# Optimization experiments

Hardware: AMD Instinct MI355X
Metric: run time of the kernel (lower is better)

Reference implementation:

```python
import jax, jax.numpy as jnp
import numpy as np

N_NODES = 50000
N_EDGES = 800000
IN_CH = 128
HID_CH = 8
OUT_CH = 64
HEADS = 32
NEG_SLOPE = 0.2  # PyG GATConv default


def setup_inputs() -> dict:
    key = jax.random.key(0)
    ks = jax.random.split(key, 12)
    x = jax.random.normal(ks[0], (N_NODES, IN_CH), dtype=jnp.float32)
    # edge_index with no self loops (src != dst), matching PyG's remove_self_loops
    src = jax.random.randint(ks[1], (N_EDGES,), 0, N_NODES)
    off = jax.random.randint(ks[2], (N_EDGES,), 1, N_NODES)
    dst = (src + off) % N_NODES
    edge_index = jnp.stack([src, dst]).astype(jnp.int64)
    s = 0.1
    W1 = jax.random.normal(ks[3], (IN_CH, HEADS * HID_CH), dtype=jnp.float32) * s
    att_src1 = jax.random.normal(ks[4], (HEADS, HID_CH), dtype=jnp.float32) * s
    att_dst1 = jax.random.normal(ks[5], (HEADS, HID_CH), dtype=jnp.float32) * s
    b1 = jnp.zeros((HEADS * HID_CH,), dtype=jnp.float32)
    W2 = jax.random.normal(ks[6], (HEADS * HID_CH, OUT_CH), dtype=jnp.float32) * s
    att_src2 = jax.random.normal(ks[7], (1, OUT_CH), dtype=jnp.float32) * s
    att_dst2 = jax.random.normal(ks[8], (1, OUT_CH), dtype=jnp.float32) * s
    b2 = jnp.zeros((OUT_CH,), dtype=jnp.float32)
    return {"x": x, "edge_index": edge_index, "W1": W1, "att_src1": att_src1,
            "att_dst1": att_dst1, "b1": b1, "W2": W2, "att_src2": att_src2,
            "att_dst2": att_dst2, "b2": b2}


def _gat_conv(x, src, dst, W, a_src, a_dst, bias, concat):
    # Faithful PyG GATConv: linear -> per-edge LeakyReLU score -> segment softmax over dst -> scatter-add
    n = x.shape[0]
    H, C = a_src.shape
    h = (x @ W).reshape(n, H, C)                      # [N,H,C]
    alpha_src = jnp.sum(h * a_src, axis=-1)           # [N,H]
    alpha_dst = jnp.sum(h * a_dst, axis=-1)           # [N,H]
    e = jax.nn.leaky_relu(alpha_src[src] + alpha_dst[dst], negative_slope=NEG_SLOPE)  # [E,H]
    e_max = jax.ops.segment_max(e, dst, num_segments=n)          # every node has a self loop
    ex = jnp.exp(e - e_max[dst])
    denom = jax.ops.segment_sum(ex, dst, num_segments=n)
    alpha = ex / (denom[dst] + 1e-16)                 # [E,H]
    msg = h[src] * alpha[:, :, None]                  # [E,H,C]
    out = jax.ops.segment_sum(msg, dst, num_segments=n)          # [N,H,C]
    out = out.reshape(n, H * C) if concat else out.mean(axis=1)
    return out + bias


def reference(x, edge_index, W1, att_src1, att_dst1, b1, W2, att_src2, att_dst2, b2):
    n = x.shape[0]
    loops = jnp.arange(n, dtype=edge_index.dtype)
    src = jnp.concatenate([edge_index[0], loops])     # add_self_loops (PyG default)
    dst = jnp.concatenate([edge_index[1], loops])
    h = _gat_conv(x, src, dst, W1, att_src1, att_dst1, b1, concat=True)
    h = _gat_conv(h, src, dst, W2, att_src2, att_dst2, b2, concat=False)
    return jax.nn.sigmoid(h)
```

## Files before the change

### kernel.cpp

```cpp
#include <hip/hip_runtime.h>
#include <hip/hip_bf16.h>

constexpr int N  = 50000;
constexpr int E  = 800000;
constexpr int F0 = 128;
constexpr int H1 = 32;
constexpr int F1 = 256;
constexpr int F2 = 64;
constexpr int NB = (N + 255) / 256;
constexpr int NPAD = 782 * 64;
constexpr int W1SZ = F0 * F1;
constexpr int W2SZ = F1 * F2;
constexpr int VA1SZ = 64 * F0;
constexpr int VA2SZ = 16 * F1;
constexpr int PREPB = (W1SZ + W2SZ + VA1SZ + VA2SZ) / 256;
constexpr int INITB = PREPB + NB;
constexpr int GB1 = NPAD / 64;
constexpr int CB  = (E + 255) / 256;
constexpr float NEG_SLOPE = 0.2f;

typedef unsigned short u16;
typedef unsigned int   u32;
typedef __attribute__((ext_vector_type(8))) short bf16x8;
typedef __attribute__((ext_vector_type(4))) float f32x4;
typedef __attribute__((ext_vector_type(2))) float f32x2;

__device__ __forceinline__ float leaky(float e) {
    return fmaxf(e, 0.f) + NEG_SLOPE * fminf(e, 0.f);
}
__device__ __forceinline__ float bf2f(u16 u) {
    u32 v = ((u32)u) << 16;
    return __builtin_bit_cast(float, v);
}
__device__ __forceinline__ u16 f2bf(float f) {
    u32 u = __builtin_bit_cast(u32, f);
    u += 0x7fffu + ((u >> 16) & 1u);
    return (u16)(u >> 16);
}
__device__ __forceinline__ u32 pack2(float a, float b) {
    return (u32)f2bf(a) | ((u32)f2bf(b) << 16);
}
__device__ __forceinline__ f32x2 up2v(u32 v) {
    f32x2 r;
    r.x = __builtin_bit_cast(float, v << 16);
    r.y = __builtin_bit_cast(float, v & 0xffff0000u);
    return r;
}

__device__ __forceinline__ int is64_check(const void* ei) {
    const unsigned long long* p = (const unsigned long long*)ei;
    unsigned long long v = p[threadIdx.x & 63];
    return __all(v < (unsigned long long)N) ? 1 : 0;
}
__device__ __forceinline__ int load_idx(const void* ei, long long i, int is64) {
    return is64 ? (int)((const long long*)ei)[i] : ((const int*)ei)[i];
}

__global__ __launch_bounds__(256) void k_init(
        const float* __restrict__ W1, const float* __restrict__ W2,
        const float* __restrict__ as1, const float* __restrict__ ad1,
        const float* __restrict__ a2s, const float* __restrict__ a2d,
        u16* __restrict__ w1t, u16* __restrict__ w2t,
        u16* __restrict__ va1t, u16* __restrict__ va2t, int* __restrict__ deg) {
    int b = blockIdx.x;
    if (b >= PREPB) {
        int i = (b - PREPB) * 256 + threadIdx.x;
        if (i < N) deg[i] = 0;
        return;
    }
    int i = b * 256 + threadIdx.x;
    if (i < W1SZ) {
        int n = i >> 7, k = i & 127;
        w1t[(n << 7) + (k ^ ((n & 7) << 3))] = f2bf(W1[k * F1 + n]);
    } else if (i < W1SZ + W2SZ) {
        int j = i - W1SZ;
        int n = j >> 8, k = j & 255;
        w2t[(n << 8) + (k ^ ((n & 7) << 3))] = f2bf(W2[k * F2 + n]);
    } else if (i < W1SZ + W2SZ + VA1SZ) {
        int j = i - W1SZ - W2SZ;
        int c = j >> 7, k = j & 127;
        const float* a = (c < 32) ? as1 : ad1;
        int h = c & 31;
        float s = 0.f;
#pragma unroll
        for (int cc = 0; cc < 8; cc++) s += W1[k * F1 + h * 8 + cc] * a[h * 8 + cc];
        va1t[(c << 7) + (k ^ ((c & 7) << 3))] = f2bf(s);
    } else if (i < W1SZ + W2SZ + VA1SZ + VA2SZ) {
        int j = i - W1SZ - W2SZ - VA1SZ;
        int jj = j >> 8, k = j & 255;
        float s = 0.f;
        if (jj < 2) {
            const float* a = jj ? a2d : a2s;
            for (int c = 0; c < 64; c++) s += W2[k * F2 + c] * a[c];
        }
        va2t[(jj << 8) + (k ^ ((jj & 7) << 3))] = f2bf(s);
    }
}

__global__ __launch_bounds__(256) void k_gemm1count(
        const float* __restrict__ x, const u16* __restrict__ w1t,
        const u16* __restrict__ va1t, const float* __restrict__ b1,
        u16* __restrict__ h1b, u16* __restrict__ asrc1b, u16* __restrict__ adst1b,
        const void* __restrict__ ei, int* __restrict__ deg) {
    if (blockIdx.x >= GB1) {
        int is64 = is64_check(ei);
        int e = (blockIdx.x - GB1) * 256 + threadIdx.x;
        if (e < E) {
            int dst = load_idx(ei, (long long)E + e, is64);
            atomicAdd(&deg[dst], 1);
        }
        return;
    }
    __shared__ u16 As[64 * 128];
    int r0 = blockIdx.x * 64;
    int t = threadIdx.x, w = t >> 6, l = t & 63;
    {
        int r = t >> 2, k0 = (t & 3) * 32, rr = r0 + r;
        int swz = (r & 7) << 3;
        float4 f[8];
        if (rr < N) {
            const float4* px = (const float4*)(x + (size_t)rr * F0 + k0);
#pragma unroll
            for (int j = 0; j < 8; j++) f[j] = px[j];
        } else {
#pragma unroll
            for (int j = 0; j < 8; j++) f[j] = make_float4(0.f, 0.f, 0.f, 0.f);
        }
#pragma unroll
        for (int g = 0; g < 4; g++) {
            uint4 st;
            st.x = pack2(f[2 * g].x, f[2 * g].y);
            st.y = pack2(f[2 * g].z, f[2 * g].w);
            st.z = pack2(f[2 * g + 1].x, f[2 * g + 1].y);
            st.w = pack2(f[2 * g + 1].z, f[2 * g + 1].w);
            *(uint4*)(As + r * 128 + ((k0 + 8 * g) ^ swz)) = st;
        }
    }
    bf16x8 bfrag[4][4];
    float b1v[4];
#pragma unroll
    for (int n = 0; n < 4; n++) {
        int col = w * 64 + n * 16 + (l & 15);
        b1v[n] = b1[col];
        const u16* wrow = w1t + col * 128;
        int swz = (col & 7) << 3;
#pragma unroll
        for (int ks = 0; ks < 4; ks++)
            bfrag[n][ks] = *(const bf16x8*)(wrow + ((ks * 32 + (l >> 4) * 8) ^ swz));
    }
    __syncthreads();
    f32x4 z = {0.f, 0.f, 0.f, 0.f};
    f32x4 acc[4][4], acc5[4];
#pragma unroll
    for (int m = 0; m < 4; m++) {
        acc5[m] = z;
#pragma unroll
        for (int n = 0; n < 4; n++) acc[m][n] = z;
    }
    int c5 = w * 16 + (l & 15);
    const u16* varow = va1t + c5 * 128;
    int swz5 = (c5 & 7) << 3;
#pragma unroll
    for (int ks = 0; ks < 4; ks++) {
        bf16x8 b5 = *(const bf16x8*)(varow + ((ks * 32 + (l >> 4) * 8) ^ swz5));
#pragma unroll
        for (int m = 0; m < 4; m++) {
            int row = m * 16 + (l & 15);
            bf16x8 a = *(const bf16x8*)(As + row * 128 +
                                        ((ks * 32 + (l >> 4) * 8) ^ ((row & 7) << 3)));
#pragma unroll
            for (int n = 0; n < 4; n++)
                acc[m][n] = __builtin_amdgcn_mfma_f32_16x16x32_bf16(a, bfrag[n][ks], acc[m][n], 0, 0, 0);
            acc5[m] = __builtin_amdgcn_mfma_f32_16x16x32_bf16(a, b5, acc5[m], 0, 0, 0);
        }
    }
#pragma unroll
    for (int m = 0; m < 4; m++) {
        int rbase = r0 + m * 16 + (l >> 4) * 4;
#pragma unroll
        for (int n = 0; n < 4; n++) {
            int col = w * 64 + n * 16 + (l & 15);
#pragma unroll
            for (int r = 0; r < 4; r++) {
                int rr = rbase + r;
                if (rr < N)
                    h1b[(size_t)rr * 256 + (col ^ ((rr & 7) << 3))] = f2bf(acc[m][n][r] + b1v[n]);
            }
        }
#pragma unroll
        for (int r = 0; r < 4; r++) {
            int rr = rbase + r;
            if (rr < N) {
                u16 v = f2bf(acc5[m][r]);
                if (c5 < 32) asrc1b[(size_t)rr * H1 + c5] = v;
                else         adst1b[(size_t)rr * H1 + (c5 - 32)] = v;
            }
        }
    }
}

__global__ __launch_bounds__(256) void k_bsum(const int* __restrict__ deg, int* __restrict__ bsum) {
    int b = blockIdx.x, t = threadIdx.x, i = b * 256 + t;
    int v = (i < N) ? deg[i] : 0;
#pragma unroll
    for (int o = 1; o < 64; o <<= 1) v += __shfl_xor(v, o, 64);
    __shared__ int sw[4];
    if ((t & 63) == 0) sw[t >> 6] = v;
    __syncthreads();
    if (t == 0) bsum[b] = sw[0] + sw[1] + sw[2] + sw[3];
}

__global__ __launch_bounds__(256) void k_rs2(
        const int* __restrict__ deg, const int* __restrict__ bsum,
        int* __restrict__ rs, int* __restrict__ rs2) {
    __shared__ int sb[NB];
    __shared__ int wtot[4];
    __shared__ int wtot2[4];
    int b = blockIdx.x, t = threadIdx.x, lane = t & 63, wy = t >> 6;
    int v = (t < NB) ? bsum[t] : 0;
    int inc = v;
#pragma unroll
    for (int o = 1; o < 64; o <<= 1) { int u = __shfl_up(inc, o, 64); if (lane >= o) inc += u; }
    if (lane == 63) wtot[wy] = inc;
    __syncthreads();
    int offs = 0;
    for (int k = 0; k < wy; k++) offs += wtot[k];
    if (t < NB) sb[t] = offs + inc - v;
    if (b == 0 && t == NB - 1) rs[N] = offs + inc;
    __syncthreads();
    int base = sb[b];
    int i = b * 256 + t;
    int dv = (i < N) ? deg[i] : 0;
    int dinc = dv;
#pragma unroll
    for (int o = 1; o < 64; o <<= 1) { int u = __shfl_up(dinc, o, 64); if (lane >= o) dinc += u; }
    if (lane == 63) wtot2[wy] = dinc;
    __syncthreads();
    int o2 = base;
    for (int k = 0; k < wy; k++) o2 += wtot2[k];
    if (i < N) {
        int e = o2 + dinc - dv;
        rs[i] = e;
        rs2[i] = e;
    }
}

__global__ void k_scatter(const void* __restrict__ ei,
                          int* __restrict__ rs2, int* __restrict__ csr) {
    int is64 = is64_check(ei);
    int e = blockIdx.x * blockDim.x + threadIdx.x;
    if (e >= E) return;
    int src = load_idx(ei, e, is64);
    int dst = load_idx(ei, (long long)E + e, is64);
    int pos = atomicAdd(&rs2[dst], 1);
    csr[pos] = src;
}

__global__ __launch_bounds__(256) void k_edge1(
        const int* __restrict__ rs, const int* __restrict__ csr,
        const u16* __restrict__ h1b, const u16* __restrict__ asrcb,
        const u16* __restrict__ adstb, u16* __restrict__ outb) {
    int d = blockIdx.x * 4 + (threadIdx.x >> 6);
    if (d >= N) return;
    int l = threadIdx.x & 63;
    int half = l >> 5, h = l & 31;
    int beg = rs[d], end = rs[d + 1];
    float adh = bf2f(adstb[(size_t)d * H1 + h]);
    float wself = __expf(leaky(bf2f(asrcb[(size_t)d * H1 + h]) + adh));
    float w0 = half ? 0.f : wself;
    float den = w0;
    f32x2 c0, c1, c2, c3;
    {
        uint4 vd = *(const uint4*)(h1b + (size_t)d * 256 + 8 * (h ^ (d & 7)));
        c0 = up2v(vd.x) * w0;
        c1 = up2v(vd.y) * w0;
        c2 = up2v(vd.z) * w0;
        c3 = up2v(vd.w) * w0;
    }
    const uint4 z4 = {0u, 0u, 0u, 0u};
    for (int i0 = beg; i0 < end; i0 += 16) {
        int s[8]; u16 avu[8]; uint4 v[8];
#pragma unroll
        for (int k = 0; k < 8; k++) {
            int i = i0 + 2 * k + half;
            s[k] = (i < end) ? csr[i] : -1;
        }
#pragma unroll
        for (int k = 0; k < 8; k++) {
            avu[k] = 0; v[k] = z4;
            if (s[k] >= 0) {
                avu[k] = asrcb[(size_t)s[k] * H1 + h];
                v[k] = *(const uint4*)(h1b + (size_t)s[k] * 256 + 8 * (h ^ (s[k] & 7)));
            }
        }
#pragma unroll
        for (int k = 0; k < 8; k++) {
            float wv = (s[k] >= 0) ? __expf(leaky(bf2f(avu[k]) + adh)) : 0.f;
            den += wv;
            f32x2 w2v = {wv, wv};
            c0 = __builtin_elementwise_fma(up2v(v[k].x), w2v, c0);
            c1 = __builtin_elementwise_fma(up2v(v[k].y), w2v, c1);
            c2 = __builtin_elementwise_fma(up2v(v[k].z), w2v, c2);
            c3 = __builtin_elementwise_fma(up2v(v[k].w), w2v, c3);
        }
    }
    den += __shfl_xor(den, 32, 64);
    c0.x += __shfl_xor(c0.x, 32, 64); c0.y += __shfl_xor(c0.y, 32, 64);
    c1.x += __shfl_xor(c1.x, 32, 64); c1.y += __shfl_xor(c1.y, 32, 64);
    c2.x += __shfl_xor(c2.x, 32, 64); c2.y += __shfl_xor(c2.y, 32, 64);
    c3.x += __shfl_xor(c3.x, 32, 64); c3.y += __shfl_xor(c3.y, 32, 64);
    if (!half) {
        float inv = 1.f / (den + 1e-16f);
        uint4 st;
        st.x = pack2(c0.x * inv, c0.y * inv);
        st.y = pack2(c1.x * inv, c1.y * inv);
        st.z = pack2(c2.x * inv, c2.y * inv);
        st.w = pack2(c3.x * inv, c3.y * inv);
        *(uint4*)(outb + (size_t)d * 256 + 8 * (h ^ (d & 7))) = st;
    }
}

__global__ __launch_bounds__(256) void k_gemm2(
        const u16* __restrict__ ab, const u16* __restrict__ w2t,
        const u16* __restrict__ va2t, const float* __restrict__ b2,
        u16* __restrict__ h2b, float* __restrict__ asrc2, float* __restrict__ adst2) {
    __shared__ u16 As[64 * 256];
    int r0 = blockIdx.x * 64;
    int t = threadIdx.x, w = t >> 6, l = t & 63;
    {
        const u16* gsrc = ab + (size_t)r0 * 256;
        int wbase = t & ~63;
#pragma unroll
        for (int i = 0; i < 8; i++) {
            __builtin_amdgcn_global_load_lds(
                (const __attribute__((address_space(1))) void*)(gsrc + (size_t)(i * 256 + t) * 8),
                (__attribute__((address_space(3))) void*)(As + (i * 256 + wbase) * 8),
                16, 0, 0);
        }
    }
    __syncthreads();
    f32x4 z = {0.f, 0.f, 0.f, 0.f};
    f32x4 acc[4], acc5 = z;
#pragma unroll
    for (int n = 0; n < 4; n++) acc[n] = z;
    int row = w * 16 + (l & 15);
    int swzA = (row & 7) << 3;
    int j5 = l & 15;
    int swz5 = (j5 & 7) << 3;
#pragma unroll
    for (int ks = 0; ks < 8; ks++) {
        int ka = ks * 32 + (l >> 4) * 8;
        bf16x8 a = *(const bf16x8*)(As + row * 256 + (ka ^ swzA));
#pragma unroll
        for (int n = 0; n < 4; n++) {
            int col = n * 16 + (l & 15);
            bf16x8 b = *(const bf16x8*)(w2t + col * 256 + (ka ^ ((col & 7) << 3)));
            acc[n] = __builtin_amdgcn_mfma_f32_16x16x32_bf16(a, b, acc[n], 0, 0, 0);
        }
        bf16x8 b5 = *(const bf16x8*)(va2t + j5 * 256 + (ka ^ swz5));
        acc5 = __builtin_amdgcn_mfma_f32_16x16x32_bf16(a, b5, acc5, 0, 0, 0);
    }
#pragma unroll
    for (int n = 0; n < 4; n++) {
        int col = n * 16 + (l & 15);
        float b2v = b2[col];
#pragma unroll
        for (int r = 0; r < 4; r++) {
            int rr = r0 + w * 16 + (l >> 4) * 4 + r;
            if (rr < N) h2b[(size_t)rr * F2 + col] = f2bf(acc[n][r] + b2v);
        }
    }
#pragma unroll
    for (int r = 0; r < 4; r++) {
        int rr = r0 + w * 16 + (l >> 4) * 4 + r;
        if (rr < N) {
            if (j5 == 0) asrc2[rr] = acc5[r];
            else if (j5 == 1) adst2[rr] = acc5[r];
        }
    }
}

__global__ __launch_bounds__(256) void k_edge2(
        const int* __restrict__ rs, const int* __restrict__ csr,
        const u16* __restrict__ h2b, const float* __restrict__ asrc,
        const float* __restrict__ adst, float* __restrict__ out) {
    int d = blockIdx.x * 4 + (threadIdx.x >> 6);
    if (d >= N) return;
    int l = threadIdx.x & 63;
    int q = l >> 3, c8 = (l & 7) * 8;
    int beg = rs[d], end = rs[d + 1];
    float add_ = adst[d];
    float wself = __expf(leaky(asrc[d] + add_));
    float w0 = (q == 0) ? wself : 0.f;
    float den = w0;
    f32x2 c0, c1, c2, c3;
    {
        uint4 vd = *(const uint4*)(h2b + (size_t)d * F2 + c8);
        c0 = up2v(vd.x) * w0;
        c1 = up2v(vd.y) * w0;
        c2 = up2v(vd.z) * w0;
        c3 = up2v(vd.w) * w0;
    }
    const uint4 z4 = {0u, 0u, 0u, 0u};
    for (int i0 = beg; i0 < end; i0 += 32) {
        int s[4]; float av[4]; uint4 v[4];
#pragma unroll
        for (int k = 0; k < 4; k++) {
            int i = i0 + 8 * k + q;
            s[k] = (i < end) ? csr[i] : -1;
        }
#pragma unroll
        for (int k = 0; k < 4; k++) {
            av[k] = 0.f; v[k] = z4;
            if (s[k] >= 0) {
                av[k] = asrc[s[k]];
                v[k] = *(const uint4*)(h2b + (size_t)s[k] * F2 + c8);
            }
        }
#pragma unroll
        for (int k = 0; k < 4; k++) {
            float wv = (s[k] >= 0) ? __expf(leaky(av[k] + add_)) : 0.f;
            den += wv;
            f32x2 w2v = {wv, wv};
            c0 = __builtin_elementwise_fma(up2v(v[k].x), w2v, c0);
            c1 = __builtin_elementwise_fma(up2v(v[k].y), w2v, c1);
            c2 = __builtin_elementwise_fma(up2v(v[k].z), w2v, c2);
            c3 = __builtin_elementwise_fma(up2v(v[k].w), w2v, c3);
        }
    }
#pragma unroll
    for (int o = 8; o < 64; o <<= 1) {
        den += __shfl_xor(den, o, 64);
        c0.x += __shfl_xor(c0.x, o, 64); c0.y += __shfl_xor(c0.y, o, 64);
        c1.x += __shfl_xor(c1.x, o, 64); c1.y += __shfl_xor(c1.y, o, 64);
        c2.x += __shfl_xor(c2.x, o, 64); c2.y += __shfl_xor(c2.y, o, 64);
        c3.x += __shfl_xor(c3.x, o, 64); c3.y += __shfl_xor(c3.y, o, 64);
    }
    if (q == 0) {
        float inv = 1.f / (den + 1e-16f);
        float4 o1, o2;
        o1.x = 1.f / (1.f + __expf(-(c0.x * inv)));
        o1.y = 1.f / (1.f + __expf(-(c0.y * inv)));
        o1.z = 1.f / (1.f + __expf(-(c1.x * inv)));
        o1.w = 1.f / (1.f + __expf(-(c1.y * inv)));
        o2.x = 1.f / (1.f + __expf(-(c2.x * inv)));
        o2.y = 1.f / (1.f + __expf(-(c2.y * inv)));
        o2.z = 1.f / (1.f + __expf(-(c3.x * inv)));
        o2.w = 1.f / (1.f + __expf(-(c3.y * inv)));
        *(float4*)(out + (size_t)d * F2 + c8) = o1;
        *(float4*)(out + (size_t)d * F2 + c8 + 4) = o2;
    }
}

extern "C" void kernel_launch(void* const* d_in, const int* in_sizes, int n_in,
                              void* d_out, int out_size, void* d_ws, size_t ws_size,
                              hipStream_t stream) {
    const float* x   = (const float*)d_in[0];
    const void*  ei  = d_in[1];
    const float* W1  = (const float*)d_in[2];
    const float* as1 = (const float*)d_in[3];
    const float* ad1 = (const float*)d_in[4];
    const float* b1  = (const float*)d_in[5];
    const float* W2  = (const float*)d_in[6];
    const float* a2s = (const float*)d_in[7];
    const float* a2d = (const float*)d_in[8];
    const float* b2  = (const float*)d_in[9];
    float* out = (float*)d_out;

    char* wp = (char*)d_ws;
    size_t off = 0;
    auto alloc = [&](size_t bytes) {
        void* p = wp + off;
        off = (off + bytes + 255) & ~(size_t)255;
        return p;
    };
    int* deg   = (int*)alloc((size_t)N * 4);
    int* rs    = (int*)alloc((size_t)(N + 1) * 4);
    int* rs2   = (int*)alloc((size_t)N * 4);
    int* bsum  = (int*)alloc((size_t)NB * 4);
    int* csr   = (int*)alloc((size_t)E * 4);
    u16* w1t   = (u16*)alloc((size_t)W1SZ * 2);
    u16* w2t   = (u16*)alloc((size_t)W2SZ * 2);
    u16* va1t  = (u16*)alloc((size_t)VA1SZ * 2);
    u16* va2t  = (u16*)alloc((size_t)VA2SZ * 2);
    u16* h1b   = (u16*)alloc((size_t)NPAD * F1 * 2);
    u16* h1ab  = (u16*)alloc((size_t)NPAD * F1 * 2);
    u16* h2b   = (u16*)alloc((size_t)NPAD * F2 * 2);
    u16* asrc1b = (u16*)alloc((size_t)N * H1 * 2);
    u16* adst1b = (u16*)alloc((size_t)N * H1 * 2);
    float* asrc2 = (float*)alloc((size_t)N * 4);
    float* adst2 = (float*)alloc((size_t)N * 4);

    k_init<<<INITB, 256, 0, stream>>>(W1, W2, as1, ad1, a2s, a2d,
                                      w1t, w2t, va1t, va2t, deg);
    k_gemm1count<<<GB1 + CB, 256, 0, stream>>>(x, w1t, va1t, b1, h1b,
                                               asrc1b, adst1b, ei, deg);
    k_bsum<<<NB, 256, 0, stream>>>(deg, bsum);
    k_rs2<<<NB, 256, 0, stream>>>(deg, bsum, rs, rs2);
    k_scatter<<<CB, 256, 0, stream>>>(ei, rs2, csr);
    k_edge1<<<(N + 3) / 4, 256, 0, stream>>>(rs, csr, h1b, asrc1b, adst1b, h1ab);
    k_gemm2<<<GB1, 256, 0, stream>>>(h1ab, w2t, va2t, b2, h2b, asrc2, adst2);
    k_edge2<<<(N + 3) / 4, 256, 0, stream>>>(rs, csr, h2b, asrc2, adst2, out);
}
```

Baseline: 230.4 us.

## Fuse CSR build kernels into one cooperative kernel with grid syncs

Merges the block-sum, prefix-scan and edge-scatter kernels into a single cooperative launch of 1024 blocks that uses grid-wide syncs between phases and grid-stride loops. This removes two kernel launch boundaries and their inter-kernel gaps. In exchange it adds grid barrier cost and caps scatter parallelism at a fixed grid size, and it relies on all 1024 blocks being co-resident for the cooperative launch.

```diff
diff --git a/kernel.cpp b/kernel.cpp
--- a/kernel.cpp
+++ b/kernel.cpp
@@ -1,5 +1,8 @@
 #include <hip/hip_runtime.h>
 #include <hip/hip_bf16.h>
+#include <hip/hip_cooperative_groups.h>
+
+namespace cg = cooperative_groups;
 
 constexpr int N  = 50000;
 constexpr int E  = 800000;
@@ -17,6 +20,7 @@
 constexpr int INITB = PREPB + NB;
 constexpr int GB1 = NPAD / 64;
 constexpr int CB  = (E + 255) / 256;
+constexpr int CSRB = 1024;
 constexpr float NEG_SLOPE = 0.2f;
 
 typedef unsigned short u16;
@@ -199,61 +203,64 @@
     }
 }
 
-__global__ __launch_bounds__(256) void k_bsum(const int* __restrict__ deg, int* __restrict__ bsum) {
-    int b = blockIdx.x, t = threadIdx.x, i = b * 256 + t;
-    int v = (i < N) ? deg[i] : 0;
-#pragma unroll
-    for (int o = 1; o < 64; o <<= 1) v += __shfl_xor(v, o, 64);
+__global__ __launch_bounds__(256) void k_csr(
+        const void* __restrict__ ei, const int* __restrict__ deg,
+        int* __restrict__ bsum, int* __restrict__ rs,
+        int* __restrict__ rs2, int* __restrict__ csr) {
+    cg::grid_group grid = cg::this_grid();
+    int t = threadIdx.x, lane = t & 63, wy = t >> 6;
     __shared__ int sw[4];
-    if ((t & 63) == 0) sw[t >> 6] = v;
-    __syncthreads();
-    if (t == 0) bsum[b] = sw[0] + sw[1] + sw[2] + sw[3];
-}
-
-__global__ __launch_bounds__(256) void k_rs2(
-        const int* __restrict__ deg, const int* __restrict__ bsum,
-        int* __restrict__ rs, int* __restrict__ rs2) {
-    __shared__ int sb[NB];
-    __shared__ int wtot[4];
-    __shared__ int wtot2[4];
-    int b = blockIdx.x, t = threadIdx.x, lane = t & 63, wy = t >> 6;
-    int v = (t < NB) ? bsum[t] : 0;
-    int inc = v;
-#pragma unroll
-    for (int o = 1; o < 64; o <<= 1) { int u = __shfl_up(inc, o, 64); if (lane >= o) inc += u; }
-    if (lane == 63) wtot[wy] = inc;
-    __syncthreads();
-    int offs = 0;
-    for (int k = 0; k < wy; k++) offs += wtot[k];
-    if (t < NB) sb[t] = offs + inc - v;
-    if (b == 0 && t == NB - 1) rs[N] = offs + inc;
-    __syncthreads();
-    int base = sb[b];
-    int i = b * 256 + t;
-    int dv = (i < N) ? deg[i] : 0;
-    int dinc = dv;
-#pragma unroll
-    for (int o = 1; o < 64; o <<= 1) { int u = __shfl_up(dinc, o, 64); if (lane >= o) dinc += u; }
-    if (lane == 63) wtot2[wy] = dinc;
-    __syncthreads();
-    int o2 = base;
-    for (int k = 0; k < wy; k++) o2 += wtot2[k];
-    if (i < N) {
-        int e = o2 + dinc - dv;
-        rs[i] = e;
-        rs2[i] = e;
-    }
-}
-
-__global__ void k_scatter(const void* __restrict__ ei,
-                          int* __restrict__ rs2, int* __restrict__ csr) {
+    for (int b = blockIdx.x; b < NB; b += gridDim.x) {
+        int i = b * 256 + t;
+        int v = (i < N) ? deg[i] : 0;
+#pragma unroll
+        for (int o = 1; o < 64; o <<= 1) v += __shfl_xor(v, o, 64);
+        if (lane == 0) sw[wy] = v;
+        __syncthreads();
+        if (t == 0) bsum[b] = sw[0] + sw[1] + sw[2] + sw[3];
+        __syncthreads();
+    }
+    grid.sync();
+    {
+        __shared__ int sb[NB];
+        __shared__ int wtot[4], wtot2[4];
+        int v = (t < NB) ? bsum[t] : 0;
+        int inc = v;
+#pragma unroll
+        for (int o = 1; o < 64; o <<= 1) { int u = __shfl_up(inc, o, 64); if (lane >= o) inc += u; }
+        if (lane == 63) wtot[wy] = inc;
+        __syncthreads();
+        int offs = 0;
+        for (int k = 0; k < wy; k++) offs += wtot[k];
+        if (t < NB) sb[t] = offs + inc - v;
+        if (blockIdx.x == 0 && t == NB - 1) rs[N] = offs + inc;
+        __syncthreads();
+        for (int b = blockIdx.x; b < NB; b += gridDim.x) {
+            int i = b * 256 + t;
+            int dv = (i < N) ? deg[i] : 0;
+            int dinc = dv;
+#pragma unroll
+            for (int o = 1; o < 64; o <<= 1) { int u = __shfl_up(dinc, o, 64); if (lane >= o) dinc += u; }
+            if (lane == 63) wtot2[wy] = dinc;
+            __syncthreads();
+            int o2 = sb[b];
+            for (int k = 0; k < wy; k++) o2 += wtot2[k];
+            if (i < N) {
+                int e0 = o2 + dinc - dv;
+                rs[i] = e0;
+                rs2[i] = e0;
+            }
+            __syncthreads();
+        }
+    }
+    grid.sync();
     int is64 = is64_check(ei);
-    int e = blockIdx.x * blockDim.x + threadIdx.x;
-    if (e >= E) return;
-    int src = load_idx(ei, e, is64);
-    int dst = load_idx(ei, (long long)E + e, is64);
-    int pos = atomicAdd(&rs2[dst], 1);
-    csr[pos] = src;
+    for (int e = blockIdx.x * 256 + t; e < E; e += gridDim.x * 256) {
+        int src = load_idx(ei, e, is64);
+        int dst = load_idx(ei, (long long)E + e, is64);
+        int pos = atomicAdd(&rs2[dst], 1);
+        csr[pos] = src;
+    }
 }
 
 __global__ __launch_bounds__(256) void k_edge1(
@@ -495,9 +502,12 @@
                                       w1t, w2t, va1t, va2t, deg);
     k_gemm1count<<<GB1 + CB, 256, 0, stream>>>(x, w1t, va1t, b1, h1b,
                                                asrc1b, adst1b, ei, deg);
-    k_bsum<<<NB, 256, 0, stream>>>(deg, bsum);
-    k_rs2<<<NB, 256, 0, stream>>>(deg, bsum, rs, rs2);
-    k_scatter<<<CB, 256, 0, stream>>>(ei, rs2, csr);
+    {
+        void* cargs[] = {(void*)&ei, (void*)&deg, (void*)&bsum,
+                         (void*)&rs, (void*)&rs2, (void*)&csr};
+        hipLaunchCooperativeKernel((void*)k_csr, dim3(CSRB), dim3(256),
+                                   cargs, 0, stream);
+    }
     k_edge1<<<(N + 3) / 4, 256, 0, stream>>>(rs, csr, h1b, asrc1b, adst1b, h1ab);
     k_gemm2<<<GB1, 256, 0, stream>>>(h1ab, w2t, va2t, b2, h2b, asrc2, adst2);
     k_edge2<<<(N + 3) / 4, 256, 0, stream>>>(rs, csr, h2b, asrc2, adst2, out);
```

Result: slower. 401.9 us (+74.4%).
